# Kernel optimization log

Hardware: AMD Instinct MI355X
Metric: run time of the kernel (lower is better)

Reference implementation:

```python
import jax, jax.numpy as jnp
import numpy as np

D = 1024
H = 16
HD = D // H


def setup_inputs() -> dict:
    key = jax.random.key(0)
    k1, k2, k3 = jax.random.split(key, 3)
    x = jax.random.normal(k1, (4, 2048, D), dtype=jnp.float32)
    # torch Linear weight is [out, in]; we store transposed [in, out] for x @ W
    w_qkv = jax.random.normal(k2, (D, 3 * D), dtype=jnp.float32) * (1.0 / np.sqrt(D))
    w_o = jax.random.normal(k3, (D, D), dtype=jnp.float32) * (1.0 / np.sqrt(D))
    return {"x": x, "w_qkv": w_qkv, "w_o": w_o}


def reference(x, w_qkv, w_o):
    B, T, _ = x.shape
    qkv = x @ w_qkv                                  # [B, T, 3D]
    q, k, v = jnp.split(qkv, 3, axis=-1)
    def heads(t):
        return t.reshape(B, T, H, HD).transpose(0, 2, 1, 3)  # [B, H, T, hd]
    q, k, v = heads(q), heads(k), heads(v)
    scale = 1.0 / jnp.sqrt(jnp.asarray(HD, x.dtype))
    att = jnp.einsum("bhtd,bhsd->bhts", q, k) * scale       # [B, H, T, T]
    att = jax.nn.softmax(att, axis=-1)
    y = jnp.einsum("bhts,bhsd->bhtd", att, v)                # [B, H, T, hd]
    y = y.transpose(0, 2, 1, 3).reshape(B, T, D)
    return y @ w_o
```

## Files before the change

### kernel.cpp

```cpp
#include <hip/hip_runtime.h>
#include <hip/hip_bf16.h>
#include <stdint.h>

typedef __attribute__((ext_vector_type(8))) short short8;
typedef __attribute__((ext_vector_type(4))) float f32x4;

#define MFMA_BF16(a, b, c) __builtin_amdgcn_mfma_f32_16x16x32_bf16((a), (b), (c), 0, 0, 0)

#define QSCALE 0.18033688011118293f

__device__ __forceinline__ unsigned short f2bf(float f) {
  unsigned int u = __builtin_bit_cast(unsigned int, f);
  u += 0x7fffu + ((u >> 16) & 1u);
  return (unsigned short)(u >> 16);
}

__device__ __forceinline__ uint32_t pkbf(float a, float b) {
  float2 f; f.x = a; f.y = b;
  __hip_bfloat162 h = __float22bfloat162_rn(f);
  uint32_t u;
  __builtin_memcpy(&u, &h, 4);
  return u;
}

__device__ __forceinline__ float exp2_fast(float x) {
#if __has_builtin(__builtin_amdgcn_exp2f)
  return __builtin_amdgcn_exp2f(x);
#else
  float r;
  asm("v_exp_f32 %0, %1" : "=v"(r) : "v"(x));
  return r;
#endif
}

__device__ __forceinline__ void gload_lds16(const void* g, void* l) {
  __builtin_amdgcn_global_load_lds(
      (const __attribute__((address_space(1))) unsigned int*)g,
      (__attribute__((address_space(3))) unsigned int*)l, 16, 0, 0);
}

__global__ __launch_bounds__(256) void cvt_f32_bf16_k(const float* __restrict__ in,
                                                      unsigned short* __restrict__ out,
                                                      int n8) {
  int i = blockIdx.x * 256 + threadIdx.x;
  if (i >= n8) return;
  const float4* p = (const float4*)(in + (size_t)i * 8);
  float4 a = p[0], b = p[1];
  short8 o;
  o[0] = (short)f2bf(a.x); o[1] = (short)f2bf(a.y);
  o[2] = (short)f2bf(a.z); o[3] = (short)f2bf(a.w);
  o[4] = (short)f2bf(b.x); o[5] = (short)f2bf(b.y);
  o[6] = (short)f2bf(b.z); o[7] = (short)f2bf(b.w);
  *(short8*)(out + (size_t)i * 8) = o;
}

__global__ __launch_bounds__(256) void transpose_f32_bf16_k(const float* __restrict__ in,
                                                            unsigned short* __restrict__ out,
                                                            int R, int C) {
  __shared__ __attribute__((aligned(16))) unsigned short t[64][65];
  int c0 = blockIdx.x * 64, r0 = blockIdx.y * 64;
  int tx = threadIdx.x;
  for (int rr = threadIdx.y; rr < 64; rr += 4)
    t[rr][tx] = f2bf(in[(size_t)(r0 + rr) * C + c0 + tx]);
  __syncthreads();
  for (int rr = threadIdx.y; rr < 64; rr += 4)
    out[(size_t)(c0 + rr) * R + r0 + tx] = t[tx][rr];
}

template <int MODE>
__global__ __launch_bounds__(256) void gemm_bt_k(
    const unsigned short* __restrict__ A, const unsigned short* __restrict__ Bt,
    float* __restrict__ Cout, unsigned short* __restrict__ Qd,
    unsigned short* __restrict__ Kd, unsigned short* __restrict__ Vtd,
    int M, int N, int Kdim) {
  __shared__ __attribute__((aligned(16))) unsigned short As[128 * 32];
  __shared__ __attribute__((aligned(16))) unsigned short Bs[128 * 32];
  const int tid = threadIdx.x, lane = tid & 63, w = tid >> 6;
  const int wr = w >> 1, wc = w & 1;
  const int lo = lane & 15, hi = lane >> 4;
  const int tm = blockIdx.y, tn = blockIdx.x;
  f32x4 acc[4][4] = {};
  const char* Ab = (const char*)A;
  const char* Bb = (const char*)Bt;
  const int nk = Kdim >> 5;
  for (int kt = 0; kt < nk; ++kt) {
    __syncthreads();
#pragma unroll
    for (int j = 0; j < 2; ++j) {
      int o8 = w * 2048 + j * 1024 + lane * 16;
      int row = o8 >> 6, cb = o8 & 63;
      gload_lds16(Ab + ((size_t)(tm * 128 + row) * Kdim + kt * 32) * 2 + cb,
                  (char*)As + w * 2048 + j * 1024);
      gload_lds16(Bb + ((size_t)(tn * 128 + row) * Kdim + kt * 32) * 2 + cb,
                  (char*)Bs + w * 2048 + j * 1024);
    }
    __syncthreads();
    short8 af[4], bf[4];
#pragma unroll
    for (int m = 0; m < 4; ++m)
      af[m] = *(const short8*)&As[(wr * 64 + m * 16 + lo) * 32 + hi * 8];
#pragma unroll
    for (int n = 0; n < 4; ++n)
      bf[n] = *(const short8*)&Bs[(wc * 64 + n * 16 + lo) * 32 + hi * 8];
#pragma unroll
    for (int m = 0; m < 4; ++m)
#pragma unroll
      for (int n = 0; n < 4; ++n)
        acc[m][n] = MFMA_BF16(af[m], bf[n], acc[m][n]);
  }
  if (MODE == 1) {
#pragma unroll
    for (int m = 0; m < 4; ++m)
#pragma unroll
      for (int n = 0; n < 4; ++n)
#pragma unroll
        for (int j = 0; j < 4; ++j) {
          int row = tm * 128 + wr * 64 + m * 16 + hi * 4 + j;
          int col = tn * 128 + wc * 64 + n * 16 + lo;
          Cout[(size_t)row * N + col] = acc[m][n][j];
        }
  } else {
    int which = (tn * 128) >> 10;
#pragma unroll
    for (int m = 0; m < 4; ++m)
#pragma unroll
      for (int n = 0; n < 4; ++n)
#pragma unroll
        for (int j = 0; j < 4; ++j) {
          int row = tm * 128 + wr * 64 + m * 16 + hi * 4 + j;
          int col = tn * 128 + wc * 64 + n * 16 + lo;
          int b = row >> 11, t = row & 2047;
          int rem = col & 1023;
          int h = rem >> 6, hd = rem & 63;
          float v = acc[m][n][j];
          if (which == 0)
            Qd[((size_t)(b * 16 + h) * 2048 + t) * 64 + hd] = f2bf(v * QSCALE);
          else if (which == 1)
            Kd[((size_t)(b * 16 + h) * 2048 + t) * 64 + hd] = f2bf(v);
          else
            Vtd[((size_t)(b * 16 + h) * 64 + hd) * 2048 + t] = f2bf(v);
        }
  }
}

__global__ __launch_bounds__(512) void attn_k(const unsigned short* __restrict__ Qd,
                                              const unsigned short* __restrict__ Kd,
                                              const unsigned short* __restrict__ Vtd,
                                              unsigned short* __restrict__ Y) {
  const int T = 2048;
  int bh = blockIdx.y, qt = blockIdx.x;
  int tid = threadIdx.x, lane = tid & 63, w = tid >> 6;
  int lo = lane & 15, hi = lane >> 4;
  const unsigned short* Qbh = Qd + (size_t)bh * T * 64;
  const char* Kb = (const char*)(Kd + (size_t)bh * T * 64);
  const char* Vb = (const char*)(Vtd + (size_t)bh * 64 * T);

  __shared__ __attribute__((aligned(16))) unsigned short Ks[2][4096];
  __shared__ __attribute__((aligned(16))) unsigned short Vs[2][4096];
  __shared__ __attribute__((aligned(16))) unsigned short Ps[8][2][1152];
  __shared__ __attribute__((aligned(16))) float fl[8][2][16];

  const short8 ones = {0x3F80, 0x3F80, 0x3F80, 0x3F80,
                       0x3F80, 0x3F80, 0x3F80, 0x3F80};

  short8 qf[2][2];
#pragma unroll
  for (int qh = 0; qh < 2; ++qh) {
    const unsigned short* qrow =
        Qbh + (size_t)(qt * 256 + w * 32 + qh * 16 + lo) * 64 + hi * 8;
    qf[qh][0] = *(const short8*)qrow;
    qf[qh][1] = *(const short8*)(qrow + 32);
  }
  f32x4 oacc[2][4] = {};
  f32x4 lacc[2] = {};
  float mrow[2] = {-1e30f, -1e30f};

#define STAGE(kt, b)                                                          \
  {                                                                           \
    int base = w * 1024;                                                      \
    int o8 = base + lane * 16;                                                \
    int src = o8 ^ (((o8 >> 7) & 7) << 4);                                    \
    gload_lds16(Kb + (size_t)(kt) * 8192 + src, (char*)Ks[b] + base);         \
    int hd_ = src >> 7, cbyt = src & 127;                                     \
    gload_lds16(Vb + (size_t)hd_ * (T * 2) + (size_t)(kt) * 128 + cbyt,       \
                (char*)Vs[b] + base);                                         \
  }

  STAGE(0, 0);
  __syncthreads();
  int buf = 0;
  for (int kt = 0; kt < T / 64; ++kt) {
    if (kt + 1 < T / 64) STAGE(kt + 1, buf ^ 1);

    f32x4 sacc[2][4] = {};
    __builtin_amdgcn_s_setprio(1);
#pragma unroll
    for (int st = 0; st < 4; ++st)
#pragma unroll
      for (int c = 0; c < 2; ++c) {
        int row = st * 16 + lo;
        int addr = (row * 128 + c * 64 + hi * 16) ^ ((row & 7) << 4);
        short8 kf = *(const short8*)((const char*)Ks[buf] + addr);
        sacc[0][st] = MFMA_BF16(kf, qf[0][c], sacc[0][st]);
        sacc[1][st] = MFMA_BF16(kf, qf[1][c], sacc[1][st]);
      }
    __builtin_amdgcn_s_setprio(0);

#pragma unroll
    for (int qh = 0; qh < 2; ++qh) {
      f32x4 mm = sacc[qh][0];
#pragma unroll
      for (int st = 1; st < 4; ++st)
#pragma unroll
        for (int r = 0; r < 4; ++r) mm[r] = fmaxf(mm[r], sacc[qh][st][r]);
      float mt = fmaxf(fmaxf(mm[0], mm[1]), fmaxf(mm[2], mm[3]));
      mt = fmaxf(mt, __shfl_xor(mt, 16));
      mt = fmaxf(mt, __shfl_xor(mt, 32));
      if (__any(mt > mrow[qh] + 8.0f)) {
        float mn = fmaxf(mrow[qh], mt);
        float fac = exp2_fast(mrow[qh] - mn);
        mrow[qh] = mn;
        fl[w][qh][lo] = fac;
        f32x4 f4 = *(const f32x4*)&fl[w][qh][hi * 4];
#pragma unroll
        for (int r = 0; r < 4; ++r) lacc[qh][r] *= f4[r];
#pragma unroll
        for (int n = 0; n < 4; ++n)
#pragma unroll
          for (int r = 0; r < 4; ++r) oacc[qh][n][r] *= f4[r];
      }
      float mn = mrow[qh];
      unsigned short* pw = &Ps[w][qh][0];
#pragma unroll
      for (int st = 0; st < 4; ++st) {
        float p0 = exp2_fast(sacc[qh][st][0] - mn);
        float p1 = exp2_fast(sacc[qh][st][1] - mn);
        float p2 = exp2_fast(sacc[qh][st][2] - mn);
        float p3 = exp2_fast(sacc[qh][st][3] - mn);
        *(uint32_t*)&pw[lo * 72 + st * 16 + hi * 4] = pkbf(p0, p1);
        *(uint32_t*)&pw[lo * 72 + st * 16 + hi * 4 + 2] = pkbf(p2, p3);
      }
    }

    __builtin_amdgcn_s_setprio(1);
#pragma unroll
    for (int c = 0; c < 2; ++c) {
      short8 pf0 = *(const short8*)&Ps[w][0][lo * 72 + c * 32 + hi * 8];
      short8 pf1 = *(const short8*)&Ps[w][1][lo * 72 + c * 32 + hi * 8];
      lacc[0] = MFMA_BF16(pf0, ones, lacc[0]);
      lacc[1] = MFMA_BF16(pf1, ones, lacc[1]);
#pragma unroll
      for (int n = 0; n < 4; ++n) {
        int row = n * 16 + lo;
        int addr = (row * 128 + c * 64 + hi * 16) ^ ((row & 7) << 4);
        short8 vf = *(const short8*)((const char*)Vs[buf] + addr);
        oacc[0][n] = MFMA_BF16(pf0, vf, oacc[0][n]);
        oacc[1][n] = MFMA_BF16(pf1, vf, oacc[1][n]);
      }
    }
    __builtin_amdgcn_s_setprio(0);
    __syncthreads();
    buf ^= 1;
  }

  int b = bh >> 4, h = bh & 15;
#pragma unroll
  for (int qh = 0; qh < 2; ++qh)
#pragma unroll
    for (int r = 0; r < 4; ++r) {
      int t = qt * 256 + w * 32 + qh * 16 + hi * 4 + r;
      float rl = 1.0f / lacc[qh][r];
#pragma unroll
      for (int n = 0; n < 4; ++n) {
        int hd = n * 16 + lo;
        Y[((size_t)(b * 2048 + t)) * 1024 + h * 64 + hd] =
            f2bf(oacc[qh][n][r] * rl);
      }
    }
}

extern "C" void kernel_launch(void* const* d_in, const int* in_sizes, int n_in,
                              void* d_out, int out_size, void* d_ws, size_t ws_size,
                              hipStream_t stream) {
  const float* x = (const float*)d_in[0];
  const float* w_qkv = (const float*)d_in[1];
  const float* w_o = (const float*)d_in[2];
  float* out = (float*)d_out;
  char* ws = (char*)d_ws;
  unsigned short* xb    = (unsigned short*)(ws + 0);
  unsigned short* wqkvT = (unsigned short*)(ws + 16777216);
  unsigned short* woT   = (unsigned short*)(ws + 23068672);
  unsigned short* qb    = (unsigned short*)(ws + 25165824);
  unsigned short* kb    = (unsigned short*)(ws + 41943040);
  unsigned short* vtb   = (unsigned short*)(ws + 58720256);
  unsigned short* yb    = xb;

  cvt_f32_bf16_k<<<4096, 256, 0, stream>>>(x, xb, 1048576);
  transpose_f32_bf16_k<<<dim3(48, 16), dim3(64, 4), 0, stream>>>(w_qkv, wqkvT, 1024, 3072);
  transpose_f32_bf16_k<<<dim3(16, 16), dim3(64, 4), 0, stream>>>(w_o, woT, 1024, 1024);
  gemm_bt_k<0><<<dim3(24, 64), 256, 0, stream>>>(xb, wqkvT, nullptr, qb, kb, vtb,
                                                 8192, 3072, 1024);
  attn_k<<<dim3(8, 64), 512, 0, stream>>>(qb, kb, vtb, yb);
  gemm_bt_k<1><<<dim3(8, 64), 256, 0, stream>>>(yb, woT, out, nullptr, nullptr, nullptr,
                                                8192, 1024, 1024);
}
```

Before: 243.6 us.

## Double-buffer GEMM LDS tiles, remap attention blocks, swizzle P scratch layout

After: 232.0 us. 1.05x faster.

```diff
diff --git a/kernel.cpp b/kernel.cpp
--- a/kernel.cpp
+++ b/kernel.cpp
@@ -73,8 +73,8 @@
     float* __restrict__ Cout, unsigned short* __restrict__ Qd,
     unsigned short* __restrict__ Kd, unsigned short* __restrict__ Vtd,
     int M, int N, int Kdim) {
-  __shared__ __attribute__((aligned(16))) unsigned short As[128 * 32];
-  __shared__ __attribute__((aligned(16))) unsigned short Bs[128 * 32];
+  __shared__ __attribute__((aligned(16))) unsigned short As[2][4096];
+  __shared__ __attribute__((aligned(16))) unsigned short Bs[2][4096];
   const int tid = threadIdx.x, lane = tid & 63, w = tid >> 6;
   const int wr = w >> 1, wc = w & 1;
   const int lo = lane & 15, hi = lane >> 4;
@@ -83,30 +83,40 @@
   const char* Ab = (const char*)A;
   const char* Bb = (const char*)Bt;
   const int nk = Kdim >> 5;
+
+#define GSTAGE(kt, bb)                                                        \
+  {                                                                           \
+    _Pragma("unroll") for (int j = 0; j < 2; ++j) {                           \
+      int o8 = w * 2048 + j * 1024 + lane * 16;                               \
+      int row = o8 >> 6, cb = o8 & 63;                                        \
+      gload_lds16(Ab + ((size_t)(tm * 128 + row) * Kdim + (kt) * 32) * 2 + cb,\
+                  (char*)As[bb] + w * 2048 + j * 1024);                       \
+      gload_lds16(Bb + ((size_t)(tn * 128 + row) * Kdim + (kt) * 32) * 2 + cb,\
+                  (char*)Bs[bb] + w * 2048 + j * 1024);                       \
+    }                                                                         \
+  }
+
+  GSTAGE(0, 0);
+  __syncthreads();
+  int gbuf = 0;
   for (int kt = 0; kt < nk; ++kt) {
-    __syncthreads();
-#pragma unroll
-    for (int j = 0; j < 2; ++j) {
-      int o8 = w * 2048 + j * 1024 + lane * 16;
-      int row = o8 >> 6, cb = o8 & 63;
-      gload_lds16(Ab + ((size_t)(tm * 128 + row) * Kdim + kt * 32) * 2 + cb,
-                  (char*)As + w * 2048 + j * 1024);
-      gload_lds16(Bb + ((size_t)(tn * 128 + row) * Kdim + kt * 32) * 2 + cb,
-                  (char*)Bs + w * 2048 + j * 1024);
-    }
-    __syncthreads();
+    if (kt + 1 < nk) GSTAGE(kt + 1, gbuf ^ 1);
     short8 af[4], bf[4];
 #pragma unroll
     for (int m = 0; m < 4; ++m)
-      af[m] = *(const short8*)&As[(wr * 64 + m * 16 + lo) * 32 + hi * 8];
+      af[m] = *(const short8*)&As[gbuf][(wr * 64 + m * 16 + lo) * 32 + hi * 8];
 #pragma unroll
     for (int n = 0; n < 4; ++n)
-      bf[n] = *(const short8*)&Bs[(wc * 64 + n * 16 + lo) * 32 + hi * 8];
+      bf[n] = *(const short8*)&Bs[gbuf][(wc * 64 + n * 16 + lo) * 32 + hi * 8];
+    __builtin_amdgcn_s_setprio(1);
 #pragma unroll
     for (int m = 0; m < 4; ++m)
 #pragma unroll
       for (int n = 0; n < 4; ++n)
         acc[m][n] = MFMA_BF16(af[m], bf[n], acc[m][n]);
+    __builtin_amdgcn_s_setprio(0);
+    __syncthreads();
+    gbuf ^= 1;
   }
   if (MODE == 1) {
 #pragma unroll
@@ -148,7 +158,9 @@
                                               const unsigned short* __restrict__ Vtd,
                                               unsigned short* __restrict__ Y) {
   const int T = 2048;
-  int bh = blockIdx.y, qt = blockIdx.x;
+  int flat = blockIdx.x;
+  int qt = (flat >> 3) & 7;
+  int bh = (flat & 7) * 8 + (flat >> 6);
   int tid = threadIdx.x, lane = tid & 63, w = tid >> 6;
   int lo = lane & 15, hi = lane >> 4;
   const unsigned short* Qbh = Qd + (size_t)bh * T * 64;
@@ -157,7 +169,7 @@
 
   __shared__ __attribute__((aligned(16))) unsigned short Ks[2][4096];
   __shared__ __attribute__((aligned(16))) unsigned short Vs[2][4096];
-  __shared__ __attribute__((aligned(16))) unsigned short Ps[8][2][1152];
+  __shared__ __attribute__((aligned(16))) unsigned short Ps[8][2][1024];
   __shared__ __attribute__((aligned(16))) float fl[8][2][16];
 
   const short8 ones = {0x3F80, 0x3F80, 0x3F80, 0x3F80,
@@ -230,23 +242,25 @@
           for (int r = 0; r < 4; ++r) oacc[qh][n][r] *= f4[r];
       }
       float mn = mrow[qh];
-      unsigned short* pw = &Ps[w][qh][0];
+      char* pw = (char*)&Ps[w][qh][0];
 #pragma unroll
       for (int st = 0; st < 4; ++st) {
         float p0 = exp2_fast(sacc[qh][st][0] - mn);
         float p1 = exp2_fast(sacc[qh][st][1] - mn);
         float p2 = exp2_fast(sacc[qh][st][2] - mn);
         float p3 = exp2_fast(sacc[qh][st][3] - mn);
-        *(uint32_t*)&pw[lo * 72 + st * 16 + hi * 4] = pkbf(p0, p1);
-        *(uint32_t*)&pw[lo * 72 + st * 16 + hi * 4 + 2] = pkbf(p2, p3);
+        int wb = (lo * 128 + st * 32 + hi * 8) ^ ((lo & 7) << 4);
+        *(uint32_t*)(pw + wb) = pkbf(p0, p1);
+        *(uint32_t*)(pw + wb + 4) = pkbf(p2, p3);
       }
     }
 
     __builtin_amdgcn_s_setprio(1);
 #pragma unroll
     for (int c = 0; c < 2; ++c) {
-      short8 pf0 = *(const short8*)&Ps[w][0][lo * 72 + c * 32 + hi * 8];
-      short8 pf1 = *(const short8*)&Ps[w][1][lo * 72 + c * 32 + hi * 8];
+      int pb = (lo * 128 + c * 64 + hi * 16) ^ ((lo & 7) << 4);
+      short8 pf0 = *(const short8*)((const char*)&Ps[w][0][0] + pb);
+      short8 pf1 = *(const short8*)((const char*)&Ps[w][1][0] + pb);
       lacc[0] = MFMA_BF16(pf0, ones, lacc[0]);
       lacc[1] = MFMA_BF16(pf1, ones, lacc[1]);
 #pragma unroll
@@ -300,7 +314,7 @@
   transpose_f32_bf16_k<<<dim3(16, 16), dim3(64, 4), 0, stream>>>(w_o, woT, 1024, 1024);
   gemm_bt_k<0><<<dim3(24, 64), 256, 0, stream>>>(xb, wqkvT, nullptr, qb, kb, vtb,
                                                  8192, 3072, 1024);
-  attn_k<<<dim3(8, 64), 512, 0, stream>>>(qb, kb, vtb, yb);
+  attn_k<<<512, 512, 0, stream>>>(qb, kb, vtb, yb);
   gemm_bt_k<1><<<dim3(8, 64), 256, 0, stream>>>(yb, woT, out, nullptr, nullptr, nullptr,
                                                 8192, 1024, 1024);
 }
```
